# Kernel optimization log

Measured on AMD Instinct MI355X. Metric: run time of the kernel, lower is better.

Reference implementation:

```python
import jax, jax.numpy as jnp
import numpy as np

KQ = 512
NEG = -1e9


def setup_inputs() -> dict:
    key = jax.random.key(0)
    k1, k2, k3, k4, k5 = jax.random.split(key, 5)
    B, NQ, NK, D, V, O = 16, 1024, 2048, 512, 512, 256
    return {
        "keys": jax.random.normal(k1, (B, NK, D), dtype=jnp.float32),
        "queries": jax.random.normal(k2, (B, NQ, D), dtype=jnp.float32),
        "values": jax.random.normal(k3, (B, NK, V), dtype=jnp.float32),
        "mask": jax.random.randint(k4, (B, NQ, NK), 0, 2, dtype=jnp.int32),
        "W_resize": jax.random.normal(k5, (O, V), dtype=jnp.float32) * (1.0 / np.sqrt(V)),
        "b_resize": jnp.zeros((O,), dtype=jnp.float32),
    }


def reference(keys, queries, values, mask, W_resize, b_resize):
    # score: scaled dot product  [B, NQ, NK]
    logits = jnp.einsum("bqd,bkd->bqk", queries, keys) / jnp.sqrt(jnp.float32(KQ))
    logits = jnp.where(mask == 0, jnp.float32(NEG), logits)
    attn = jax.nn.softmax(logits, axis=-1)
    # context: [B, NQ, V]
    context = jnp.einsum("bqk,bkv->bqv", attn, values)
    # resize to out_size
    context = jnp.einsum("bqv,ov->bqo", context, W_resize) + b_resize
    return context
```

## Files before the change

kernel.cpp:

```cpp
#include <hip/hip_runtime.h>

#define BB   16
#define NQ   1024
#define NK   2048
#define DD   512
#define VV   512
#define OO   256
#define SCALE 0.044194173824159216f

typedef __attribute__((ext_vector_type(4))) float f32x4;
typedef __attribute__((ext_vector_type(8))) short s16x8;

#define AS1(p) ((const __attribute__((address_space(1))) void*)(p))
#define AS3(p) ((__attribute__((address_space(3))) void*)(p))

__device__ __forceinline__ unsigned short f2bf(float f) {
  unsigned u = __float_as_uint(f);
  u += 0x7fffu + ((u >> 16) & 1u);
  return (unsigned short)(u >> 16);
}
__device__ __forceinline__ float bf2f(unsigned short b) {
  return __uint_as_float(((unsigned)b) << 16);
}

#define MFMA16(a, b, c) __builtin_amdgcn_mfma_f32_16x16x32_bf16(a, b, c, 0, 0, 0)

__device__ __forceinline__ void gemm_bt_core(
    const unsigned short* __restrict__ Abase,
    const unsigned short* __restrict__ Bbase,
    int K,
    unsigned short* As, unsigned short* Bs,
    f32x4 acc[4][4])
{
  const int t = threadIdx.x;
  const int w = t >> 6;
  const int l = t & 63;
  const int srow = l >> 2;
  const int scol = (l & 3) * 8;
  const int r0 = (w * 2 + 0) * 16 + srow;
  const int r1 = (w * 2 + 1) * 16 + srow;
  const int lds0 = (w * 2 + 0) * 512 + l * 8;
  const int lds1 = (w * 2 + 1) * 512 + l * 8;
  const int wm = (w >> 1) * 64;
  const int wn = (w & 1) * 64;
  const int lm = l & 15;
  const int lq = l >> 4;

  for (int kt = 0; kt < K; kt += 32) {
    __builtin_amdgcn_global_load_lds(AS1(Abase + (size_t)r0 * K + kt + scol), AS3(As + lds0), 16, 0, 0);
    __builtin_amdgcn_global_load_lds(AS1(Abase + (size_t)r1 * K + kt + scol), AS3(As + lds1), 16, 0, 0);
    __builtin_amdgcn_global_load_lds(AS1(Bbase + (size_t)r0 * K + kt + scol), AS3(Bs + lds0), 16, 0, 0);
    __builtin_amdgcn_global_load_lds(AS1(Bbase + (size_t)r1 * K + kt + scol), AS3(Bs + lds1), 16, 0, 0);
    __syncthreads();
    s16x8 af[4], bfr[4];
    #pragma unroll
    for (int i = 0; i < 4; ++i) {
      af[i]  = *(const s16x8*)(As + (wm + i * 16 + lm) * 32 + lq * 8);
      bfr[i] = *(const s16x8*)(Bs + (wn + i * 16 + lm) * 32 + lq * 8);
    }
    #pragma unroll
    for (int mi = 0; mi < 4; ++mi)
      #pragma unroll
      for (int ni = 0; ni < 4; ++ni)
        acc[mi][ni] = MFMA16(af[mi], bfr[ni], acc[mi][ni]);
    __syncthreads();
  }
}


#define CS_STRIDE 136

__global__ __launch_bounds__(256)
void qkvw_kernel(const unsigned short* __restrict__ Qb,
                 const unsigned short* __restrict__ Kb,
                 const unsigned short* __restrict__ Vb,
                 const unsigned short* __restrict__ Wb,
                 const int* __restrict__ mask,
                 unsigned short* __restrict__ P,
                 unsigned short* __restrict__ VWt)
{
  __shared__ unsigned short smem[128 * CS_STRIDE];
  unsigned short* As = smem;
  unsigned short* Bs = smem + 4096;
  unsigned short* Cs = smem;
  const int bid0 = blockIdx.x;
  const int bid = (bid0 & 7) * 320 + (bid0 >> 3);
  const int t = threadIdx.x, w = t >> 6, l = t & 63;
  const int wm = (w >> 1) * 64, wn = (w & 1) * 64;
  const int lm = l & 15, lq = l >> 4;
  const int trow = t >> 4, tcol = (t & 15) * 8;

  f32x4 acc[4][4];
  #pragma unroll
  for (int i = 0; i < 4; ++i)
    #pragma unroll
    for (int j = 0; j < 4; ++j) acc[i][j] = (f32x4){0.f, 0.f, 0.f, 0.f};

  if (bid < 2048) {
    const int b  = bid >> 7;
    const int tm = (bid >> 4) & 7;
    const int tn = bid & 15;

    gemm_bt_core(Qb + ((size_t)b * NQ + tm * 128) * DD,
                 Kb + ((size_t)b * NK + tn * 128) * DD, DD, As, Bs, acc);

    #pragma unroll
    for (int mi = 0; mi < 4; ++mi)
      #pragma unroll
      for (int ni = 0; ni < 4; ++ni)
        #pragma unroll
        for (int r = 0; r < 4; ++r)
          Cs[(wm + mi * 16 + lq * 4 + r) * CS_STRIDE + wn + ni * 16 + lm] =
              f2bf(acc[mi][ni][r] * SCALE);
    __syncthreads();

    #pragma unroll
    for (int it = 0; it < 8; ++it) {
      const int row = it * 16 + trow;
      const int gq = tm * 128 + row;
      const size_t gbase = ((size_t)b * NQ + gq) * NK + tn * 128 + tcol;
      s16x8 v = *(const s16x8*)(Cs + row * CS_STRIDE + tcol);
      const int4 m0 = *(const int4*)(mask + gbase);
      const int4 m1 = *(const int4*)(mask + gbase + 4);
      s16x8 o;
      o[0] = m0.x ? (short)f2bf(__expf(bf2f((unsigned short)v[0]))) : (short)0;
      o[1] = m0.y ? (short)f2bf(__expf(bf2f((unsigned short)v[1]))) : (short)0;
      o[2] = m0.z ? (short)f2bf(__expf(bf2f((unsigned short)v[2]))) : (short)0;
      o[3] = m0.w ? (short)f2bf(__expf(bf2f((unsigned short)v[3]))) : (short)0;
      o[4] = m1.x ? (short)f2bf(__expf(bf2f((unsigned short)v[4]))) : (short)0;
      o[5] = m1.y ? (short)f2bf(__expf(bf2f((unsigned short)v[5]))) : (short)0;
      o[6] = m1.z ? (short)f2bf(__expf(bf2f((unsigned short)v[6]))) : (short)0;
      o[7] = m1.w ? (short)f2bf(__expf(bf2f((unsigned short)v[7]))) : (short)0;
      *(s16x8*)(P + gbase) = o;
    }
  } else {
    const int vid = bid - 2048;
    const int b  = vid >> 5;
    const int kt = (vid >> 1) & 15;
    const int ot = vid & 1;

    gemm_bt_core(Vb + ((size_t)b * NK + kt * 128) * VV,
                 Wb + (size_t)ot * 128 * VV, VV, As, Bs, acc);

    #pragma unroll
    for (int mi = 0; mi < 4; ++mi)
      #pragma unroll
      for (int ni = 0; ni < 4; ++ni)
        #pragma unroll
        for (int r = 0; r < 4; ++r)
          Cs[(wn + ni * 16 + lm) * CS_STRIDE + wm + mi * 16 + lq * 4 + r] =
              f2bf(acc[mi][ni][r]);
    __syncthreads();

    #pragma unroll
    for (int it = 0; it < 8; ++it) {
      const int orow = it * 16 + trow;
      s16x8 v = *(const s16x8*)(Cs + orow * CS_STRIDE + tcol);
      *(s16x8*)(VWt + ((size_t)b * OO + ot * 128 + orow) * NK + kt * 128 + tcol) = v;
    }
  }
}

#define PW_STRIDE 132
__global__ __launch_bounds__(256)
void pvw_kernel(const unsigned short* __restrict__ P,
                const unsigned short* __restrict__ VWt,
                const float* __restrict__ bias,
                float* __restrict__ out)
{
  const int ot = blockIdx.x;
  const int qt = blockIdx.y;
  const int b  = blockIdx.z;
  __shared__ unsigned short smem[24576];

  const int t = threadIdx.x, w = t >> 6, l = t & 63;
  const int wr = w >> 1, wc = w & 1;
  const int lm = l & 15, lq = l >> 4;

  f32x4 acc[2][4];
  #pragma unroll
  for (int i = 0; i < 2; ++i)
    #pragma unroll
    for (int j = 0; j < 4; ++j) acc[i][j] = (f32x4){0.f, 0.f, 0.f, 0.f};
  f32x4 accS[2];
  accS[0] = (f32x4){0.f, 0.f, 0.f, 0.f};
  accS[1] = (f32x4){0.f, 0.f, 0.f, 0.f};
  s16x8 ones;
  #pragma unroll
  for (int j = 0; j < 8; ++j) ones[j] = (short)0x3F80;

  const unsigned short* Abase = P   + ((size_t)b * NQ + qt * 64) * NK;
  const unsigned short* Bbase = VWt + ((size_t)b * OO + ot * 128) * NK;

  const int srow = t >> 3;
  const int ssc  = (((t & 7) ^ (srow & 7)) << 3);

#define PV_STAGE(buf, k0v) do {                                                            \
    unsigned short* As_ = smem + (buf) * 12288;                                            \
    unsigned short* Bs_ = As_ + 4096;                                                      \
    const int k0_ = (k0v);                                                                 \
    __builtin_amdgcn_global_load_lds(AS1(Abase + (size_t)(srow     ) * NK + k0_ + ssc), AS3(As_ +        t * 8), 16, 0, 0); \
    __builtin_amdgcn_global_load_lds(AS1(Abase + (size_t)(srow + 32) * NK + k0_ + ssc), AS3(As_ + 2048 + t * 8), 16, 0, 0); \
    __builtin_amdgcn_global_load_lds(AS1(Bbase + (size_t)(srow     ) * NK + k0_ + ssc), AS3(Bs_ +        t * 8), 16, 0, 0); \
    __builtin_amdgcn_global_load_lds(AS1(Bbase + (size_t)(srow + 32) * NK + k0_ + ssc), AS3(Bs_ + 2048 + t * 8), 16, 0, 0); \
    __builtin_amdgcn_global_load_lds(AS1(Bbase + (size_t)(srow + 64) * NK + k0_ + ssc), AS3(Bs_ + 4096 + t * 8), 16, 0, 0); \
    __builtin_amdgcn_global_load_lds(AS1(Bbase + (size_t)(srow + 96) * NK + k0_ + ssc), AS3(Bs_ + 6144 + t * 8), 16, 0, 0); \
  } while (0)

  PV_STAGE(0, 0);
  __syncthreads();
  for (int k0 = 0; k0 < NK; k0 += 64) {
    const int cur = (k0 >> 6) & 1;
    if (k0 + 64 < NK) PV_STAGE(cur ^ 1, k0 + 64);
    const unsigned short* As = smem + cur * 12288;
    const unsigned short* Bs = As + 4096;
    s16x8 af[2][2], bfr[4][2];
    #pragma unroll
    for (int mi = 0; mi < 2; ++mi) {
      const int row = wr * 32 + mi * 16 + lm;
      #pragma unroll
      for (int ks = 0; ks < 2; ++ks)
        af[mi][ks] = *(const s16x8*)(As + row * 64 + (((ks * 4 + lq) ^ (row & 7)) << 3));
    }
    #pragma unroll
    for (int ni = 0; ni < 4; ++ni) {
      const int row = wc * 64 + ni * 16 + lm;
      #pragma unroll
      for (int ks = 0; ks < 2; ++ks)
        bfr[ni][ks] = *(const s16x8*)(Bs + row * 64 + (((ks * 4 + lq) ^ (row & 7)) << 3));
    }
    #pragma unroll
    for (int mi = 0; mi < 2; ++mi) {
      #pragma unroll
      for (int ni = 0; ni < 4; ++ni) {
        acc[mi][ni] = MFMA16(af[mi][0], bfr[ni][0], acc[mi][ni]);
        acc[mi][ni] = MFMA16(af[mi][1], bfr[ni][1], acc[mi][ni]);
      }
      accS[mi] = MFMA16(af[mi][0], ones, accS[mi]);
      accS[mi] = MFMA16(af[mi][1], ones, accS[mi]);
    }
    __syncthreads();
  }
#undef PV_STAGE

  float* Csf = (float*)smem;
  #pragma unroll
  for (int mi = 0; mi < 2; ++mi)
    #pragma unroll
    for (int r = 0; r < 4; ++r) {
      const float inv = 1.0f / accS[mi][r];
      const int row = wr * 32 + mi * 16 + lq * 4 + r;
      #pragma unroll
      for (int ni = 0; ni < 4; ++ni) {
        const int col = wc * 64 + ni * 16 + lm;
        Csf[row * PW_STRIDE + col] = acc[mi][ni][r] * inv;
      }
    }
  __syncthreads();
  const int trow = t >> 2;
  #pragma unroll
  for (int it = 0; it < 4; ++it) {
    const int col = (t & 3) * 8 + it * 32;
    f32x4 a = *(const f32x4*)(Csf + trow * PW_STRIDE + col);
    f32x4 c = *(const f32x4*)(Csf + trow * PW_STRIDE + col + 4);
    const int go = ot * 128 + col;
    a += *(const f32x4*)(bias + go);
    c += *(const f32x4*)(bias + go + 4);
    float* o = out + ((size_t)b * NQ + qt * 64 + trow) * OO + go;
    *(f32x4*)o = a;
    *(f32x4*)(o + 4) = c;
  }
}

__device__ __forceinline__ void cvt8(const float* __restrict__ in,
                                     unsigned short* __restrict__ out, int i)
{
  const float4* p = (const float4*)in + (size_t)i * 2;
  const float4 a = p[0], b = p[1];
  s16x8 o;
  o[0] = (short)f2bf(a.x); o[1] = (short)f2bf(a.y);
  o[2] = (short)f2bf(a.z); o[3] = (short)f2bf(a.w);
  o[4] = (short)f2bf(b.x); o[5] = (short)f2bf(b.y);
  o[6] = (short)f2bf(b.z); o[7] = (short)f2bf(b.w);
  ((s16x8*)out)[i] = o;
}

__global__ __launch_bounds__(256)
void prep_kernel(const float* __restrict__ q, const float* __restrict__ k,
                 const float* __restrict__ v, const float* __restrict__ w,
                 unsigned short* __restrict__ Qb, unsigned short* __restrict__ Kb,
                 unsigned short* __restrict__ Vb, unsigned short* __restrict__ Wb)
{
  const int bid = blockIdx.x;
  const int t = threadIdx.x;
  if (bid < 4096) {
    cvt8(q, Qb, bid * 256 + t);
  } else if (bid < 12288) {
    cvt8(k, Kb, (bid - 4096) * 256 + t);
  } else if (bid < 20480) {
    cvt8(v, Vb, (bid - 12288) * 256 + t);
  } else {
    cvt8(w, Wb, (bid - 20480) * 256 + t);
  }
}

extern "C" void kernel_launch(void* const* d_in, const int* in_sizes, int n_in,
                              void* d_out, int out_size, void* d_ws, size_t ws_size,
                              hipStream_t stream)
{
  const float* keys    = (const float*)d_in[0];
  const float* queries = (const float*)d_in[1];
  const float* values  = (const float*)d_in[2];
  const int*   mask    = (const int*)  d_in[3];
  const float* W       = (const float*)d_in[4];
  const float* bias    = (const float*)d_in[5];
  float* out = (float*)d_out;

  char* ws = (char*)d_ws;
  unsigned short* Qb  = (unsigned short*)(ws);
  unsigned short* Kb  = (unsigned short*)(ws + (16ull << 20));
  unsigned short* Vb  = (unsigned short*)(ws + (48ull << 20));
  unsigned short* Wb  = (unsigned short*)(ws + (80ull << 20));
  unsigned short* VWt = (unsigned short*)(ws + (81ull << 20));
  unsigned short* P   = (unsigned short*)(ws + (97ull << 20));

  prep_kernel<<<dim3(20544), 256, 0, stream>>>(queries, keys, values, W,
                                               Qb, Kb, Vb, Wb);
  qkvw_kernel<<<dim3(2560), 256, 0, stream>>>(Qb, Kb, Vb, Wb, mask, P, VWt);
  pvw_kernel<<<dim3(OO / 128, NQ / 64, BB), 256, 0, stream>>>(P, VWt, bias, out);
}
```

Before: 413.8 us.

## Shrink PVW query tile to 32 rows and make prep kernel grid-stride

The PV·W kernel now processes 32 query rows per block instead of 64, with each of the four waves owning a 32-column slice of the 128 output columns. This doubles the block count and cuts LDS use per block, trading more redundant loads of the VWt tile per query row for better occupancy and CU coverage. The prep conversion kernel moves from one block per chunk with branching to a fixed 2048-block grid where each thread converts several chunks of Q, K, V and W, which reduces launch and block-scheduling overhead.

```diff
diff --git a/kernel.cpp b/kernel.cpp
--- a/kernel.cpp
+++ b/kernel.cpp
@@ -171,17 +171,16 @@
   const int ot = blockIdx.x;
   const int qt = blockIdx.y;
   const int b  = blockIdx.z;
-  __shared__ unsigned short smem[24576];
+  __shared__ unsigned short smem[20480];
 
   const int t = threadIdx.x, w = t >> 6, l = t & 63;
-  const int wr = w >> 1, wc = w & 1;
   const int lm = l & 15, lq = l >> 4;
 
-  f32x4 acc[2][4];
+  f32x4 acc[2][2];
   #pragma unroll
   for (int i = 0; i < 2; ++i)
     #pragma unroll
-    for (int j = 0; j < 4; ++j) acc[i][j] = (f32x4){0.f, 0.f, 0.f, 0.f};
+    for (int j = 0; j < 2; ++j) acc[i][j] = (f32x4){0.f, 0.f, 0.f, 0.f};
   f32x4 accS[2];
   accS[0] = (f32x4){0.f, 0.f, 0.f, 0.f};
   accS[1] = (f32x4){0.f, 0.f, 0.f, 0.f};
@@ -189,18 +188,17 @@
   #pragma unroll
   for (int j = 0; j < 8; ++j) ones[j] = (short)0x3F80;
 
-  const unsigned short* Abase = P   + ((size_t)b * NQ + qt * 64) * NK;
+  const unsigned short* Abase = P   + ((size_t)b * NQ + qt * 32) * NK;
   const unsigned short* Bbase = VWt + ((size_t)b * OO + ot * 128) * NK;
 
   const int srow = t >> 3;
   const int ssc  = (((t & 7) ^ (srow & 7)) << 3);
 
 #define PV_STAGE(buf, k0v) do {                                                            \
-    unsigned short* As_ = smem + (buf) * 12288;                                            \
-    unsigned short* Bs_ = As_ + 4096;                                                      \
+    unsigned short* As_ = smem + (buf) * 10240;                                            \
+    unsigned short* Bs_ = As_ + 2048;                                                      \
     const int k0_ = (k0v);                                                                 \
     __builtin_amdgcn_global_load_lds(AS1(Abase + (size_t)(srow     ) * NK + k0_ + ssc), AS3(As_ +        t * 8), 16, 0, 0); \
-    __builtin_amdgcn_global_load_lds(AS1(Abase + (size_t)(srow + 32) * NK + k0_ + ssc), AS3(As_ + 2048 + t * 8), 16, 0, 0); \
     __builtin_amdgcn_global_load_lds(AS1(Bbase + (size_t)(srow     ) * NK + k0_ + ssc), AS3(Bs_ +        t * 8), 16, 0, 0); \
     __builtin_amdgcn_global_load_lds(AS1(Bbase + (size_t)(srow + 32) * NK + k0_ + ssc), AS3(Bs_ + 2048 + t * 8), 16, 0, 0); \
     __builtin_amdgcn_global_load_lds(AS1(Bbase + (size_t)(srow + 64) * NK + k0_ + ssc), AS3(Bs_ + 4096 + t * 8), 16, 0, 0); \
@@ -212,19 +210,19 @@
   for (int k0 = 0; k0 < NK; k0 += 64) {
     const int cur = (k0 >> 6) & 1;
     if (k0 + 64 < NK) PV_STAGE(cur ^ 1, k0 + 64);
-    const unsigned short* As = smem + cur * 12288;
-    const unsigned short* Bs = As + 4096;
-    s16x8 af[2][2], bfr[4][2];
+    const unsigned short* As = smem + cur * 10240;
+    const unsigned short* Bs = As + 2048;
+    s16x8 af[2][2], bfr[2][2];
     #pragma unroll
     for (int mi = 0; mi < 2; ++mi) {
-      const int row = wr * 32 + mi * 16 + lm;
+      const int row = mi * 16 + lm;
       #pragma unroll
       for (int ks = 0; ks < 2; ++ks)
         af[mi][ks] = *(const s16x8*)(As + row * 64 + (((ks * 4 + lq) ^ (row & 7)) << 3));
     }
     #pragma unroll
-    for (int ni = 0; ni < 4; ++ni) {
-      const int row = wc * 64 + ni * 16 + lm;
+    for (int ni = 0; ni < 2; ++ni) {
+      const int row = w * 32 + ni * 16 + lm;
       #pragma unroll
       for (int ks = 0; ks < 2; ++ks)
         bfr[ni][ks] = *(const s16x8*)(Bs + row * 64 + (((ks * 4 + lq) ^ (row & 7)) << 3));
@@ -232,7 +230,7 @@
     #pragma unroll
     for (int mi = 0; mi < 2; ++mi) {
       #pragma unroll
-      for (int ni = 0; ni < 4; ++ni) {
+      for (int ni = 0; ni < 2; ++ni) {
         acc[mi][ni] = MFMA16(af[mi][0], bfr[ni][0], acc[mi][ni]);
         acc[mi][ni] = MFMA16(af[mi][1], bfr[ni][1], acc[mi][ni]);
       }
@@ -249,24 +247,24 @@
     #pragma unroll
     for (int r = 0; r < 4; ++r) {
       const float inv = 1.0f / accS[mi][r];
-      const int row = wr * 32 + mi * 16 + lq * 4 + r;
-      #pragma unroll
-      for (int ni = 0; ni < 4; ++ni) {
-        const int col = wc * 64 + ni * 16 + lm;
+      const int row = mi * 16 + lq * 4 + r;
+      #pragma unroll
+      for (int ni = 0; ni < 2; ++ni) {
+        const int col = w * 32 + ni * 16 + lm;
         Csf[row * PW_STRIDE + col] = acc[mi][ni][r] * inv;
       }
     }
   __syncthreads();
-  const int trow = t >> 2;
-  #pragma unroll
-  for (int it = 0; it < 4; ++it) {
-    const int col = (t & 3) * 8 + it * 32;
+  const int trow = t >> 3;
+  #pragma unroll
+  for (int it = 0; it < 2; ++it) {
+    const int col = (t & 7) * 8 + it * 64;
     f32x4 a = *(const f32x4*)(Csf + trow * PW_STRIDE + col);
     f32x4 c = *(const f32x4*)(Csf + trow * PW_STRIDE + col + 4);
     const int go = ot * 128 + col;
     a += *(const f32x4*)(bias + go);
     c += *(const f32x4*)(bias + go + 4);
-    float* o = out + ((size_t)b * NQ + qt * 64 + trow) * OO + go;
+    float* o = out + ((size_t)b * NQ + qt * 32 + trow) * OO + go;
     *(f32x4*)o = a;
     *(f32x4*)(o + 4) = c;
   }
@@ -285,23 +283,22 @@
   ((s16x8*)out)[i] = o;
 }
 
+#define PREP_NTH (2048 * 256)
+
 __global__ __launch_bounds__(256)
 void prep_kernel(const float* __restrict__ q, const float* __restrict__ k,
                  const float* __restrict__ v, const float* __restrict__ w,
                  unsigned short* __restrict__ Qb, unsigned short* __restrict__ Kb,
                  unsigned short* __restrict__ Vb, unsigned short* __restrict__ Wb)
 {
-  const int bid = blockIdx.x;
-  const int t = threadIdx.x;
-  if (bid < 4096) {
-    cvt8(q, Qb, bid * 256 + t);
-  } else if (bid < 12288) {
-    cvt8(k, Kb, (bid - 4096) * 256 + t);
-  } else if (bid < 20480) {
-    cvt8(v, Vb, (bid - 12288) * 256 + t);
-  } else {
-    cvt8(w, Wb, (bid - 20480) * 256 + t);
-  }
+  const int tid = blockIdx.x * 256 + threadIdx.x;
+  #pragma unroll
+  for (int it = 0; it < 2; ++it) cvt8(q, Qb, tid + it * PREP_NTH);
+  #pragma unroll
+  for (int it = 0; it < 4; ++it) cvt8(k, Kb, tid + it * PREP_NTH);
+  #pragma unroll
+  for (int it = 0; it < 4; ++it) cvt8(v, Vb, tid + it * PREP_NTH);
+  if (tid < 16384) cvt8(w, Wb, tid);
 }
 
 extern "C" void kernel_launch(void* const* d_in, const int* in_sizes, int n_in,
@@ -324,8 +321,8 @@
   unsigned short* VWt = (unsigned short*)(ws + (81ull << 20));
   unsigned short* P   = (unsigned short*)(ws + (97ull << 20));
 
-  prep_kernel<<<dim3(20544), 256, 0, stream>>>(queries, keys, values, W,
-                                               Qb, Kb, Vb, Wb);
+  prep_kernel<<<dim3(2048), 256, 0, stream>>>(queries, keys, values, W,
+                                              Qb, Kb, Vb, Wb);
   qkvw_kernel<<<dim3(2560), 256, 0, stream>>>(Qb, Kb, Vb, Wb, mask, P, VWt);
-  pvw_kernel<<<dim3(OO / 128, NQ / 64, BB), 256, 0, stream>>>(P, VWt, bias, out);
-}
+  pvw_kernel<<<dim3(OO / 128, NQ / 32, BB), 256, 0, stream>>>(P, VWt, bias, out);
+}
```

Measured after the change: 434.1 us. 1.05x slower.
